# Kernel tuning notes

Measured on AMD Instinct MI355X. Metric: run time of the kernel, lower is better.

Reference implementation:

```python
import jax, jax.numpy as jnp
import numpy as np

B, S, D, H = 4, 2048, 1024, 16
DK = D // H
THETA = 10000.0


def _rope(x, pos):
    # x: [..., s, d_k] interleaved-pair rotation (GPT-NeoX/torch-from-scratch style)
    half = DK // 2
    inv_freq = 1.0 / (THETA ** (jnp.arange(half, dtype=jnp.float32) * 2.0 / DK))
    ang = pos.astype(jnp.float32)[:, None] * inv_freq  # [s, half]
    cos, sin = jnp.cos(ang), jnp.sin(ang)
    x1, x2 = x[..., 0::2], x[..., 1::2]
    out = jnp.stack([x1 * cos - x2 * sin, x1 * sin + x2 * cos], axis=-1)
    return out.reshape(x.shape)


def setup_inputs() -> dict:
    key = jax.random.key(0)
    ks = jax.random.split(key, 5)
    w_scale = 1.0 / np.sqrt(D)
    return {
        "x": jax.random.normal(ks[0], (B, S, D), dtype=jnp.float32),
        "W_q": jax.random.normal(ks[1], (D, D), dtype=jnp.float32) * w_scale,
        "W_k": jax.random.normal(ks[2], (D, D), dtype=jnp.float32) * w_scale,
        "W_v": jax.random.normal(ks[3], (D, D), dtype=jnp.float32) * w_scale,
        "W_o": jax.random.normal(ks[4], (D, D), dtype=jnp.float32) * w_scale,
        "token_positions": jnp.arange(S, dtype=jnp.int32),
    }


def reference(x, W_q, W_k, W_v, W_o, token_positions):
    b, s, d = x.shape

    def proj(W):  # x @ W.T, split heads -> [b, h, s, d_k]
        y = jnp.einsum('bsd,ed->bse', x, W)
        return y.reshape(b, s, H, DK).transpose(0, 2, 1, 3)

    Q, K, V = proj(W_q), proj(W_k), proj(W_v)
    Q = _rope(Q, token_positions)
    K = _rope(K, token_positions)

    scores = jnp.einsum('bhqd,bhkd->bhqk', Q, K) / jnp.sqrt(jnp.float32(DK))
    causal = jnp.tril(jnp.ones((s, s), dtype=bool))
    scores = jnp.where(causal, scores, -jnp.inf)
    attn = jax.nn.softmax(scores, axis=-1)
    out = jnp.einsum('bhqk,bhkd->bhqd', attn, V)
    out = out.transpose(0, 2, 1, 3).reshape(b, s, d)
    return jnp.einsum('bsd,ed->bse', out, W_o)
```

## Files before the change

kernel.cpp:

```cpp
#include <hip/hip_runtime.h>
#include <stdint.h>

#define B_ 4
#define S_ 2048
#define D_ 1024
#define H_ 16
#define DK_ 64
#define M_ (B_*S_)

typedef __attribute__((ext_vector_type(8))) short short8;
typedef __attribute__((ext_vector_type(4))) float f32x4;
typedef __attribute__((ext_vector_type(16))) float f32x16;
typedef __attribute__((ext_vector_type(2))) unsigned int u32x2;

static __device__ __forceinline__ float bf2f(unsigned short s) {
  union { unsigned u; float f; } v; v.u = ((unsigned)s) << 16; return v.f;
}
static __device__ __forceinline__ unsigned short f2bf(float f) {
  union { float f; unsigned u; } v; v.f = f;
  unsigned r = v.u + 0x7fffu + ((v.u >> 16) & 1u);
  return (unsigned short)(r >> 16);
}
static __device__ __forceinline__ unsigned cvtpk_bf16(float lo, float hi) {
  unsigned r;
  asm("v_cvt_pk_bf16_f32 %0, %1, %2" : "=v"(r) : "v"(lo), "v"(hi));
  return r;
}

#define GLDS16(g, l) __builtin_amdgcn_global_load_lds( \
    (const __attribute__((address_space(1))) unsigned int*)(g), \
    (__attribute__((address_space(3))) unsigned int*)(l), 16, 0, 0)

__global__ void cvt_kernel(const float* __restrict__ in, unsigned short* __restrict__ out, int n4) {
  int i = blockIdx.x * 256 + threadIdx.x;
  float4 v = ((const float4*)in)[i];
  ushort4 o;
  o.x = f2bf(v.x); o.y = f2bf(v.y); o.z = f2bf(v.z); o.w = f2bf(v.w);
  ((ushort4*)out)[i] = o;
}

__global__ void cvt_w_kernel(const float* __restrict__ w0, const float* __restrict__ w1,
                             const float* __restrict__ w2, const float* __restrict__ w3,
                             unsigned short* __restrict__ o0, unsigned short* __restrict__ o1,
                             unsigned short* __restrict__ o2, unsigned short* __restrict__ o3) {
  int idx = blockIdx.x * 256 + threadIdx.x;
  int w = idx >> 18, i = idx & 262143;
  const float* src = (w == 0) ? w0 : (w == 1) ? w1 : (w == 2) ? w2 : w3;
  unsigned short* dst = (w == 0) ? o0 : (w == 1) ? o1 : (w == 2) ? o2 : o3;
  float4 v = ((const float4*)src)[i];
  ushort4 o;
  o.x = f2bf(v.x); o.y = f2bf(v.y); o.z = f2bf(v.z); o.w = f2bf(v.w);
  ((ushort4*)dst)[i] = o;
}

#define GEMM_BODY \
  __shared__ __align__(16) char lA[2][128*128]; \
  __shared__ __align__(16) char lB[2][128*128]; \
  int t = threadIdx.x; \
  int wave = t >> 6, lane = t & 63; \
  int ln15 = lane & 15, lgrp = lane >> 4; \
  int wr = wave >> 1, wc = wave & 1; \
  f32x4 acc[4][4]; \
  _Pragma("unroll") \
  for (int m = 0; m < 4; ++m) \
    _Pragma("unroll") \
    for (int n = 0; n < 4; ++n) { f32x4 z = {0.f,0.f,0.f,0.f}; acc[m][n] = z; } \
  const char* pA[4]; const char* pB[4]; int sdst[4]; \
  _Pragma("unroll") \
  for (int i_ = 0; i_ < 4; ++i_) { \
    int a_ = (i_*256 + t) << 4; \
    int r_ = a_ >> 7; \
    int cb_ = (a_ & 127) ^ ((r_ & 7) << 4); \
    sdst[i_] = a_; \
    pA[i_] = Ab + (size_t)r_*(K*2) + cb_; \
    pB[i_] = Bb + (size_t)r_*(K*2) + cb_; \
  } \
  GSTAGE(0); \
  __syncthreads(); \
  { int cur = 0; \
    for (int k0 = 0; k0 < K; k0 += 64) { \
      if (k0 + 64 < K) GSTAGE(cur ^ 1); \
      GEMM_COMPUTE(cur); \
      __syncthreads(); \
      cur ^= 1; \
    } }

#define GSTAGE(bufi) do { \
    _Pragma("unroll") \
    for (int i_ = 0; i_ < 4; ++i_) { \
      GLDS16(pA[i_], lA[bufi] + sdst[i_]); \
      GLDS16(pB[i_], lB[bufi] + sdst[i_]); \
      pA[i_] += 128; pB[i_] += 128; \
    } \
  } while (0)

#define GEMM_COMPUTE(bufi) do { \
    const char* cA_ = lA[bufi]; \
    const char* cB_ = lB[bufi]; \
    _Pragma("unroll") \
    for (int kf = 0; kf < 2; ++kf) { \
      int cb = kf*64 + lgrp*16; \
      short8 af[4], bfr[4]; \
      _Pragma("unroll") \
      for (int m = 0; m < 4; ++m) { \
        int r = wr*64 + m*16 + ln15; \
        af[m] = *(const short8*)(cA_ + r*128 + (cb ^ ((r & 7) << 4))); \
      } \
      _Pragma("unroll") \
      for (int n = 0; n < 4; ++n) { \
        int r = wc*64 + n*16 + ln15; \
        bfr[n] = *(const short8*)(cB_ + r*128 + (cb ^ ((r & 7) << 4))); \
      } \
      __builtin_amdgcn_s_setprio(1); \
      _Pragma("unroll") \
      for (int m = 0; m < 4; ++m) \
        _Pragma("unroll") \
        for (int n = 0; n < 4; ++n) \
          acc[m][n] = __builtin_amdgcn_mfma_f32_16x16x32_bf16(af[m], bfr[n], acc[m][n], 0, 0, 0); \
      __builtin_amdgcn_s_setprio(0); \
    } \
  } while (0)

__global__ __launch_bounds__(256) void gemm_qk(const unsigned short* __restrict__ A,
                                               const unsigned short* __restrict__ W,
                                               unsigned short* __restrict__ Qo,
                                               unsigned short* __restrict__ Ko) {
  const int K = 1024;
  int bn = blockIdx.x;
  int bm = blockIdx.y;
  const char* Ab = (const char*)A + (size_t)bm * 128 * (K*2);
  const char* Bb = (const char*)W + (size_t)bn * 128 * (K*2);
  GEMM_BODY

  unsigned short* Out = (bn < 8) ? Qo : Ko;
#pragma unroll
  for (int m = 0; m < 4; ++m)
#pragma unroll
    for (int n = 0; n < 4; ++n)
#pragma unroll
      for (int r = 0; r < 4; ++r) {
        int row = bm*128 + wr*64 + m*16 + lgrp*4 + r;
        int cc = (bn & 7)*128 + wc*64 + n*16 + ln15;
        int b = row >> 11, s = row & (S_-1);
        int h = cc >> 6, dk = cc & 63;
        Out[(((size_t)(b*H_ + h)*S_ + s) << 6) + dk] = f2bf(acc[m][n][r]);
      }
}

__global__ __launch_bounds__(256) void gemm_v(const unsigned short* __restrict__ A,
                                              const unsigned short* __restrict__ W,
                                              unsigned short* __restrict__ Vo) {
  const int K = 1024;
  int bx = blockIdx.x;
  int bm = bx >> 3, bn = bx & 7;
  const char* Ab = (const char*)A + (size_t)bm * 128 * (K*2);
  const char* Bb = (const char*)W + (size_t)bn * 128 * (K*2);
  GEMM_BODY

#pragma unroll
  for (int m = 0; m < 4; ++m)
#pragma unroll
    for (int n = 0; n < 4; ++n)
#pragma unroll
      for (int r = 0; r < 4; ++r) {
        int row = bm*128 + wr*64 + m*16 + lgrp*4 + r;
        int cc = bn*128 + wc*64 + n*16 + ln15;
        int b = row >> 11, s = row & (S_-1);
        int h = cc >> 6, dk = cc & 63;
        Vo[(((size_t)(b*H_ + h)*DK_ + dk) * S_) + s] = f2bf(acc[m][n][r]);
      }
}

__global__ __launch_bounds__(256) void gemm_out(const unsigned short* __restrict__ A,
                                                const unsigned short* __restrict__ W,
                                                float* __restrict__ Out) {
  const int K = 1024, N = 1024;
  int bx = blockIdx.x;
  int bm = bx >> 3, bn = bx & 7;
  const char* Ab = (const char*)A + (size_t)bm * 128 * (K*2);
  const char* Bb = (const char*)W + (size_t)bn * 128 * (K*2);
  GEMM_BODY

#pragma unroll
  for (int m = 0; m < 4; ++m)
#pragma unroll
    for (int n = 0; n < 4; ++n)
#pragma unroll
      for (int r = 0; r < 4; ++r) {
        int row = bm*128 + wr*64 + m*16 + lgrp*4 + r;
        int col = bn*128 + wc*64 + n*16 + ln15;
        Out[(size_t)row * N + col] = acc[m][n][r];
      }
}

__global__ void rope_kernel(unsigned short* __restrict__ Qb, unsigned short* __restrict__ Kb,
                            const int* __restrict__ pos) {
  int idx = blockIdx.x * 256 + threadIdx.x;
  int g = idx & 1048575;
  unsigned short* base = (idx >> 20) ? Kb : Qb;
  float scale = (idx >> 20) ? 1.0f : (0.125f * 1.4426950408889634f);
  int jb = g & 7;
  int s = (g >> 3) & (S_-1);
  int bh = g >> 14;
  unsigned short* p = base + (((size_t)bh * S_ + s) << 6) + jb*8;
  short8 v = *(short8*)p;
  float ps = (float)pos[s];
#pragma unroll
  for (int jj = 0; jj < 4; ++jj) {
    int j = jb*4 + jj;
    float freq = exp2f(-(float)j * (13.287712379549449f / 32.0f));
    float ang = ps * freq;
    float sn, cs;
    sincosf(ang, &sn, &cs);
    float x1 = bf2f((unsigned short)v[2*jj]), x2 = bf2f((unsigned short)v[2*jj+1]);
    v[2*jj]   = (short)f2bf((x1*cs - x2*sn) * scale);
    v[2*jj+1] = (short)f2bf((x1*sn + x2*cs) * scale);
  }
  *(short8*)p = v;
}

__global__ __launch_bounds__(256) void attn_kernel(const unsigned short* __restrict__ Q,
                                                   const unsigned short* __restrict__ Kg,
                                                   const unsigned short* __restrict__ VT,
                                                   unsigned short* __restrict__ O) {
  int bid = blockIdx.x;
  int bh = bid & 63;
  int qt = 15 - (bid >> 6);
  int b = bh >> 4, h = bh & 15;
  const int qbase = qt * 128;
  const unsigned short* Qp = Q + (((size_t)bh * S_ + qbase) << 6);
  const char* Kp = (const char*)(Kg + ((size_t)bh * S_ << 6));
  const char* Vp = (const char*)(VT + (size_t)bh * DK_ * S_);

  __shared__ __align__(16) char lK[3][64*128];
  __shared__ __align__(16) char lV[3][64*128];

  int t = threadIdx.x, wave = t >> 6, lane = t & 63;
  int ln31 = lane & 31, hi = lane >> 5;
  int qw = wave * 32;
  int qg = qbase + qw + ln31;

  short8 qf[4];
#pragma unroll
  for (int kk = 0; kk < 4; ++kk)
    qf[kk] = *(const short8*)(Qp + (size_t)(qw + ln31)*64 + kk*16 + hi*8);

  f32x16 oc[2];
#pragma unroll
  for (int dh = 0; dh < 2; ++dh)
#pragma unroll
    for (int r = 0; r < 16; ++r) oc[dh][r] = 0.f;
  float li = 0.f;

  const int nt = 2*qt + 2;

  const char* pK[2]; const char* pV[2]; int kdst[2];
#pragma unroll
  for (int i_ = 0; i_ < 2; ++i_) {
    int a_ = ((i_*256 + t) << 4);
    int r_ = a_ >> 7;
    int cb_ = (a_ & 127) ^ ((r_ & 7) << 4);
    kdst[i_] = a_;
    pK[i_] = Kp + (size_t)r_*128 + cb_;
    pV[i_] = Vp + (size_t)r_*(S_*2) + cb_;
  }
#define STAGE_KV(kbuf, vbuf) do { \
    _Pragma("unroll") \
    for (int i_ = 0; i_ < 2; ++i_) { \
      GLDS16(pK[i_], (kbuf) + kdst[i_]); \
      GLDS16(pV[i_], (vbuf) + kdst[i_]); \
      pK[i_] += 64*128; pV[i_] += 128; \
    } \
  } while (0)

  char *Ka = lK[0], *Kb_ = lK[1], *Kc = lK[2];
  char *Va = lV[0], *Vb = lV[1], *Vc = lV[2];

  STAGE_KV(Ka, Va);
  STAGE_KV(Kb_, Vb);
  asm volatile("s_waitcnt vmcnt(4)" ::: "memory");
  __builtin_amdgcn_s_barrier();

  for (int kt = 0; kt < nt; ++kt) {
    bool more = (kt + 2 < nt);
    if (more) STAGE_KV(Kc, Vc);

    const char* cK = Ka;
    const char* cV = Va;
    bool active = (kt*64 <= qbase + qw + 31);
    bool diag   = (kt*64 + 63 > qbase + qw);

    if (active) {
      f32x16 sc[2];
      __builtin_amdgcn_s_setprio(1);
#pragma unroll
      for (int t2 = 0; t2 < 2; ++t2) {
        f32x16 a;
#pragma unroll
        for (int r = 0; r < 16; ++r) a[r] = 0.f;
        int rK = t2*32 + ln31;
        int swz = (rK & 7) << 4;
#pragma unroll
        for (int kk = 0; kk < 4; ++kk) {
          short8 kfr = *(const short8*)(cK + rK*128 + ((kk*32 + hi*16) ^ swz));
          a = __builtin_amdgcn_mfma_f32_32x32x16_bf16(kfr, qf[kk], a, 0, 0, 0);
        }
        sc[t2] = a;
      }
      __builtin_amdgcn_s_setprio(0);

      if (diag) {
#pragma unroll
        for (int t2 = 0; t2 < 2; ++t2)
#pragma unroll
          for (int r = 0; r < 16; ++r) {
            int kv = kt*64 + t2*32 + (r & 3) + 8*(r >> 2) + 4*hi;
            if (kv > qg) sc[t2][r] = -__builtin_inff();
          }
      }

      float lss[4] = {0.f, 0.f, 0.f, 0.f};
#pragma unroll
      for (int t2 = 0; t2 < 2; ++t2)
#pragma unroll
        for (int r = 0; r < 16; ++r) {
          float pv = __builtin_amdgcn_exp2f(sc[t2][r]);
          sc[t2][r] = pv; lss[r & 3] += pv;
        }
      li += (lss[0] + lss[1]) + (lss[2] + lss[3]);

#pragma unroll
      for (int kk = 0; kk < 4; ++kk) {
        int base = 8*(kk & 1), tt = kk >> 1;
        unsigned P0 = cvtpk_bf16(sc[tt][base+0], sc[tt][base+1]);
        unsigned P1 = cvtpk_bf16(sc[tt][base+2], sc[tt][base+3]);
        unsigned Q0 = cvtpk_bf16(sc[tt][base+4], sc[tt][base+5]);
        unsigned Q1 = cvtpk_bf16(sc[tt][base+6], sc[tt][base+7]);
        u32x2 r01 = __builtin_amdgcn_permlane32_swap(P0, Q0, false, false);
        u32x2 s01 = __builtin_amdgcn_permlane32_swap(P1, Q1, false, false);
        union { unsigned u[4]; short8 s8; } pf;
        pf.u[0] = r01[0]; pf.u[1] = s01[0]; pf.u[2] = r01[1]; pf.u[3] = s01[1];
        __builtin_amdgcn_s_setprio(1);
#pragma unroll
        for (int dh = 0; dh < 2; ++dh) {
          int rV = dh*32 + ln31;
          short8 vfr = *(const short8*)(cV + rV*128 + (((kk*32 + hi*16)) ^ ((rV & 7) << 4)));
          oc[dh] = __builtin_amdgcn_mfma_f32_32x32x16_bf16(vfr, pf.s8, oc[dh], 0, 0, 0);
        }
        __builtin_amdgcn_s_setprio(0);
      }
    }

    if (more) asm volatile("s_waitcnt vmcnt(4)" ::: "memory");
    else      asm volatile("s_waitcnt vmcnt(0)" ::: "memory");
    __builtin_amdgcn_s_barrier();

    char* tk = Ka; Ka = Kb_; Kb_ = Kc; Kc = tk;
    char* tv = Va; Va = Vb;  Vb = Vc;  Vc = tv;
  }
#undef STAGE_KV

  float lf = li + __shfl_xor(li, 32);
  float rinv = 1.0f / lf;
#pragma unroll
  for (int dh = 0; dh < 2; ++dh)
#pragma unroll
    for (int rg = 0; rg < 4; ++rg) {
      ushort4 pk4;
      pk4.x = f2bf(oc[dh][rg*4+0] * rinv);
      pk4.y = f2bf(oc[dh][rg*4+1] * rinv);
      pk4.z = f2bf(oc[dh][rg*4+2] * rinv);
      pk4.w = f2bf(oc[dh][rg*4+3] * rinv);
      int dk = dh*32 + 8*rg + 4*hi;
      *(ushort4*)(O + (((size_t)(b*S_ + qg)) << 10) + h*64 + dk) = pk4;
    }
}

extern "C" void kernel_launch(void* const* d_in, const int* in_sizes, int n_in,
                              void* d_out, int out_size, void* d_ws, size_t ws_size,
                              hipStream_t stream) {
  const float* x  = (const float*)d_in[0];
  const float* Wq = (const float*)d_in[1];
  const float* Wk = (const float*)d_in[2];
  const float* Wv = (const float*)d_in[3];
  const float* Wo = (const float*)d_in[4];
  const int* pos  = (const int*)d_in[5];

  char* ws = (char*)d_ws;
  unsigned short* xb  = (unsigned short*)(ws + 0);
  unsigned short* wqb = (unsigned short*)(ws + 16777216);
  unsigned short* wkb = (unsigned short*)(ws + 18874368);
  unsigned short* wvb = (unsigned short*)(ws + 20971520);
  unsigned short* wob = (unsigned short*)(ws + 23068672);
  unsigned short* Qb  = (unsigned short*)(ws + 25165824);
  unsigned short* Kb  = (unsigned short*)(ws + 41943040);
  unsigned short* VTb = (unsigned short*)(ws + 58720256);
  unsigned short* Ob  = xb;

  cvt_kernel<<<8192, 256, 0, stream>>>(x, xb, 2097152);
  cvt_w_kernel<<<4096, 256, 0, stream>>>(Wq, Wk, Wv, Wo, wqb, wkb, wvb, wob);

  gemm_qk<<<dim3(16, 64), 256, 0, stream>>>(xb, wqb, Qb, Kb);
  gemm_v<<<512, 256, 0, stream>>>(xb, wvb, VTb);

  rope_kernel<<<8192, 256, 0, stream>>>(Qb, Kb, pos);

  attn_kernel<<<1024, 256, 0, stream>>>(Qb, Kb, VTb, Ob);

  gemm_out<<<512, 256, 0, stream>>>(Ob, wob, (float*)d_out);
}
```

Before: 172.3 us.

## Fuse RoPE into QK GEMM epilogue with precomputed cos/sin table

Removes the standalone RoPE pass by applying the rotation in the QK projection epilogue. Adjacent output columns are paired with a lane shuffle, and cos/sin come from a small table computed once per call. The two conversion kernels are merged into one launch. This drops a full read-modify-write of Q and K plus one launch, at the cost of extra table loads in the GEMM epilogue and reusing the V buffer region for the table before gemm_v overwrites it.

```diff
diff --git a/kernel.cpp b/kernel.cpp
--- a/kernel.cpp
+++ b/kernel.cpp
@@ -31,22 +31,31 @@
     (const __attribute__((address_space(1))) unsigned int*)(g), \
     (__attribute__((address_space(3))) unsigned int*)(l), 16, 0, 0)
 
-__global__ void cvt_kernel(const float* __restrict__ in, unsigned short* __restrict__ out, int n4) {
-  int i = blockIdx.x * 256 + threadIdx.x;
-  float4 v = ((const float4*)in)[i];
-  ushort4 o;
-  o.x = f2bf(v.x); o.y = f2bf(v.y); o.z = f2bf(v.z); o.w = f2bf(v.w);
-  ((ushort4*)out)[i] = o;
-}
-
-__global__ void cvt_w_kernel(const float* __restrict__ w0, const float* __restrict__ w1,
-                             const float* __restrict__ w2, const float* __restrict__ w3,
-                             unsigned short* __restrict__ o0, unsigned short* __restrict__ o1,
-                             unsigned short* __restrict__ o2, unsigned short* __restrict__ o3) {
+__global__ void rope_tab_kernel(const int* __restrict__ pos, float2* __restrict__ tab) {
   int idx = blockIdx.x * 256 + threadIdx.x;
-  int w = idx >> 18, i = idx & 262143;
-  const float* src = (w == 0) ? w0 : (w == 1) ? w1 : (w == 2) ? w2 : w3;
-  unsigned short* dst = (w == 0) ? o0 : (w == 1) ? o1 : (w == 2) ? o2 : o3;
+  int s = idx >> 5, j = idx & 31;
+  float freq = exp2f(-(float)j * (13.287712379549449f / 32.0f));
+  float ang = (float)pos[s] * freq;
+  float sn, cs;
+  sincosf(ang, &sn, &cs);
+  tab[idx] = make_float2(cs, sn);
+}
+
+__global__ void cvt_all_kernel(const float* __restrict__ x,
+                               const float* __restrict__ w0, const float* __restrict__ w1,
+                               const float* __restrict__ w2, const float* __restrict__ w3,
+                               unsigned short* __restrict__ xb,
+                               unsigned short* __restrict__ o0, unsigned short* __restrict__ o1,
+                               unsigned short* __restrict__ o2, unsigned short* __restrict__ o3) {
+  int idx = blockIdx.x * 256 + threadIdx.x;
+  const float* src; unsigned short* dst; int i;
+  if (idx < 2097152) { src = x; dst = xb; i = idx; }
+  else {
+    int widx = idx - 2097152;
+    int w = widx >> 18; i = widx & 262143;
+    src = (w == 0) ? w0 : (w == 1) ? w1 : (w == 2) ? w2 : w3;
+    dst = (w == 0) ? o0 : (w == 1) ? o1 : (w == 2) ? o2 : o3;
+  }
   float4 v = ((const float4*)src)[i];
   ushort4 o;
   o.x = f2bf(v.x); o.y = f2bf(v.y); o.z = f2bf(v.z); o.w = f2bf(v.w);
@@ -123,6 +132,7 @@
 
 __global__ __launch_bounds__(256) void gemm_qk(const unsigned short* __restrict__ A,
                                                const unsigned short* __restrict__ W,
+                                               const float2* __restrict__ Tab,
                                                unsigned short* __restrict__ Qo,
                                                unsigned short* __restrict__ Ko) {
   const int K = 1024;
@@ -133,6 +143,7 @@
   GEMM_BODY
 
   unsigned short* Out = (bn < 8) ? Qo : Ko;
+  float qs = (bn < 8) ? (0.125f * 1.4426950408889634f) : 1.0f;
 #pragma unroll
   for (int m = 0; m < 4; ++m)
 #pragma unroll
@@ -143,7 +154,12 @@
         int cc = (bn & 7)*128 + wc*64 + n*16 + ln15;
         int b = row >> 11, s = row & (S_-1);
         int h = cc >> 6, dk = cc & 63;
-        Out[(((size_t)(b*H_ + h)*S_ + s) << 6) + dk] = f2bf(acc[m][n][r]);
+        float v = acc[m][n][r];
+        float p = __shfl_xor(v, 1);
+        float2 cssn = Tab[(s << 5) + (dk >> 1)];
+        float sgn = (dk & 1) ? cssn.y : -cssn.y;
+        float o = (v * cssn.x + p * sgn) * qs;
+        Out[(((size_t)(b*H_ + h)*S_ + s) << 6) + dk] = f2bf(o);
       }
 }
 
@@ -191,32 +207,6 @@
         int col = bn*128 + wc*64 + n*16 + ln15;
         Out[(size_t)row * N + col] = acc[m][n][r];
       }
-}
-
-__global__ void rope_kernel(unsigned short* __restrict__ Qb, unsigned short* __restrict__ Kb,
-                            const int* __restrict__ pos) {
-  int idx = blockIdx.x * 256 + threadIdx.x;
-  int g = idx & 1048575;
-  unsigned short* base = (idx >> 20) ? Kb : Qb;
-  float scale = (idx >> 20) ? 1.0f : (0.125f * 1.4426950408889634f);
-  int jb = g & 7;
-  int s = (g >> 3) & (S_-1);
-  int bh = g >> 14;
-  unsigned short* p = base + (((size_t)bh * S_ + s) << 6) + jb*8;
-  short8 v = *(short8*)p;
-  float ps = (float)pos[s];
-#pragma unroll
-  for (int jj = 0; jj < 4; ++jj) {
-    int j = jb*4 + jj;
-    float freq = exp2f(-(float)j * (13.287712379549449f / 32.0f));
-    float ang = ps * freq;
-    float sn, cs;
-    sincosf(ang, &sn, &cs);
-    float x1 = bf2f((unsigned short)v[2*jj]), x2 = bf2f((unsigned short)v[2*jj+1]);
-    v[2*jj]   = (short)f2bf((x1*cs - x2*sn) * scale);
-    v[2*jj+1] = (short)f2bf((x1*sn + x2*cs) * scale);
-  }
-  *(short8*)p = v;
 }
 
 __global__ __launch_bounds__(256) void attn_kernel(const unsigned short* __restrict__ Q,
@@ -395,16 +385,15 @@
   unsigned short* Qb  = (unsigned short*)(ws + 25165824);
   unsigned short* Kb  = (unsigned short*)(ws + 41943040);
   unsigned short* VTb = (unsigned short*)(ws + 58720256);
+  float2* tab = (float2*)VTb;
   unsigned short* Ob  = xb;
 
-  cvt_kernel<<<8192, 256, 0, stream>>>(x, xb, 2097152);
-  cvt_w_kernel<<<4096, 256, 0, stream>>>(Wq, Wk, Wv, Wo, wqb, wkb, wvb, wob);
-
-  gemm_qk<<<dim3(16, 64), 256, 0, stream>>>(xb, wqb, Qb, Kb);
+  rope_tab_kernel<<<256, 256, 0, stream>>>(pos, tab);
+  cvt_all_kernel<<<12288, 256, 0, stream>>>(x, Wq, Wk, Wv, Wo, xb, wqb, wkb, wvb, wob);
+
+  gemm_qk<<<dim3(16, 64), 256, 0, stream>>>(xb, wqb, tab, Qb, Kb);
   gemm_v<<<512, 256, 0, stream>>>(xb, wvb, VTb);
 
-  rope_kernel<<<8192, 256, 0, stream>>>(Qb, Kb, pos);
-
   attn_kernel<<<1024, 256, 0, stream>>>(Qb, Kb, VTb, Ob);
 
   gemm_out<<<512, 256, 0, stream>>>(Ob, wob, (float*)d_out);
```

After: 167.9 us. -2.6%, faster.
